# Performance work log

Hardware: AMD Instinct MI355X
Metric: run time of the kernel (lower is better)

Reference implementation:

```python
import jax, jax.numpy as jnp
import numpy as np

NUM_HEADS = 12
HEAD_DIM = 64
EPS = 1e-5


def _ln(t, g, b):
    m = t.mean(-1, keepdims=True)
    v = ((t - m) ** 2).mean(-1, keepdims=True)
    return (t - m) * jax.lax.rsqrt(v + EPS) * g + b


def _pool(t, conv_w, g, b, B, H, W, C):
    # t: [B, heads, 1+H*W, C] -> depthwise-conv pooled [B, heads, 1+Hp*Wp, C]
    cls = t[:, :, :1, :]
    sp = t[:, :, 1:, :].reshape(B * NUM_HEADS, H, W, C).transpose(0, 3, 1, 2)
    y = jax.lax.conv_general_dilated(
        sp, conv_w, (2, 2), [(1, 1), (1, 1)],
        feature_group_count=C,
        dimension_numbers=('NCHW', 'OIHW', 'NCHW'))
    Hp, Wp = y.shape[2], y.shape[3]
    y = y.reshape(B, NUM_HEADS, C, Hp * Wp).transpose(0, 1, 3, 2)
    y = jnp.concatenate([cls, y], axis=2)
    return _ln(y, g, b), (Hp, Wp)


def _rel_dist(q_s, k_s):
    q_ratio = max(k_s / q_s, 1.0)
    k_ratio = max(q_s / k_s, 1.0)
    d = jnp.arange(q_s)[:, None] * q_ratio - jnp.arange(k_s)[None, :] * k_ratio
    d = d + (k_s - 1) * k_ratio
    return d.astype(jnp.int32)


def _forward(x, pool_q_w, pool_k_w, pool_v_w,
             norm_q_g, norm_q_b, norm_k_g, norm_k_b, norm_v_g, norm_v_b,
             wq, bq, wk, bk, wv, bv, proj_w, proj_b,
             rel_pos_h, rel_pos_w, feat_h, feat_w):
    B, N, D = x.shape
    C = D // NUM_HEADS
    t = x.reshape(B, N, NUM_HEADS, C).transpose(0, 2, 1, 3)  # [B,h,N,C]
    q, (qh, qw) = _pool(t, pool_q_w, norm_q_g, norm_q_b, B, feat_h, feat_w, C)
    k, (kh, kw) = _pool(t, pool_k_w, norm_k_g, norm_k_b, B, feat_h, feat_w, C)
    v, _ = _pool(t, pool_v_w, norm_v_g, norm_v_b, B, feat_h, feat_w, C)

    def proj_heads(y, w, bias):
        n = y.shape[2]
        y = y.transpose(0, 2, 1, 3).reshape(B, n, D)
        y = y @ w + bias
        return y.reshape(B, n, NUM_HEADS, HEAD_DIM).transpose(0, 2, 1, 3)

    q = proj_heads(q, wq, bq)
    k = proj_heads(k, wk, bk)
    v = proj_heads(v, wv, bv)

    scale = HEAD_DIM ** -0.5
    attn = jnp.einsum('bhqd,bhkd->bhqk', q * scale, k)

    # spatial relative position bias (cal_rel_pos_type), cls token excluded
    Rh = rel_pos_h[_rel_dist(qh, kh)]   # [qh,kh,hd]
    Rw = rel_pos_w[_rel_dist(qw, kw)]   # [qw,kw,hd]
    r_q = q[:, :, 1:, :].reshape(B, NUM_HEADS, qh, qw, HEAD_DIM)
    rel_h = jnp.einsum('byhwc,hkc->byhwk', r_q, Rh)
    rel_w = jnp.einsum('byhwc,wkc->byhwk', r_q, Rw)
    bias2d = (rel_h[..., :, None] + rel_w[..., None, :]).reshape(
        B, NUM_HEADS, qh * qw, kh * kw)
    attn = attn.at[:, :, 1:, 1:].add(bias2d)

    attn = jax.nn.softmax(attn, axis=-1)
    out = jnp.einsum('bhqk,bhkd->bhqd', attn, v)
    out = out + q  # residual pooling
    out = out.transpose(0, 2, 1, 3).reshape(B, -1, NUM_HEADS * HEAD_DIM)
    return out @ proj_w + proj_b


def setup_inputs() -> dict:
    key = jax.random.key(0)
    ks = jax.random.split(key, 16)
    B, D, C = 16, 768, 64
    H = W = 56
    N = H * W + 1
    rs = 2 * 28 - 1
    rnd = lambda i, sh, s: jax.random.normal(ks[i], sh, jnp.float32) * s
    return {
        'x': rnd(0, (B, N, D), 1.0),
        'pool_q_w': rnd(1, (C, 1, 3, 3), 0.1),
        'pool_k_w': rnd(2, (C, 1, 3, 3), 0.1),
        'pool_v_w': rnd(3, (C, 1, 3, 3), 0.1),
        'norm_q_g': jnp.ones((C,), jnp.float32),
        'norm_q_b': jnp.zeros((C,), jnp.float32),
        'norm_k_g': jnp.ones((C,), jnp.float32),
        'norm_k_b': jnp.zeros((C,), jnp.float32),
        'norm_v_g': jnp.ones((C,), jnp.float32),
        'norm_v_b': jnp.zeros((C,), jnp.float32),
        'wq': rnd(4, (D, D), 0.02), 'bq': jnp.zeros((D,), jnp.float32),
        'wk': rnd(5, (D, D), 0.02), 'bk': jnp.zeros((D,), jnp.float32),
        'wv': rnd(6, (D, D), 0.02), 'bv': jnp.zeros((D,), jnp.float32),
        'proj_w': rnd(7, (D, D), 0.02), 'proj_b': jnp.zeros((D,), jnp.float32),
        'rel_pos_h': rnd(8, (rs, HEAD_DIM), 0.02),
        'rel_pos_w': rnd(9, (rs, HEAD_DIM), 0.02),
        'feat_h': 56, 'feat_w': 56,
    }


def reference(x, pool_q_w, pool_k_w, pool_v_w,
              norm_q_g, norm_q_b, norm_k_g, norm_k_b, norm_v_g, norm_v_b,
              wq, bq, wk, bk, wv, bv, proj_w, proj_b,
              rel_pos_h, rel_pos_w, feat_h, feat_w):
    return _forward(x, pool_q_w, pool_k_w, pool_v_w,
                    norm_q_g, norm_q_b, norm_k_g, norm_k_b,
                    norm_v_g, norm_v_b,
                    wq, bq, wk, bk, wv, bv, proj_w, proj_b,
                    rel_pos_h, rel_pos_w, int(feat_h), int(feat_w))
```

## Files before the change

### kernel.cpp

```cpp
#include <hip/hip_runtime.h>
#include <stdint.h>

#define NUM_HEADS 12
#define HEAD_DIM  64
#define HWDIM     56
#define PHDIM     28
#define NTOK      785
#define NIN       3137
#define BATCH     16
#define DMODEL    768
#define BHCNT     192
#define LOG2E     1.44269504f

typedef __attribute__((ext_vector_type(8))) short bf16x8;
typedef __attribute__((ext_vector_type(4))) short s16x4;
typedef __attribute__((ext_vector_type(4))) float f32x4;

static __device__ __forceinline__ float bf2f(short s) {
  unsigned u = ((unsigned)(unsigned short)s) << 16;
  float f; __builtin_memcpy(&f, &u, 4); return f;
}
static __device__ __forceinline__ short f2bf(float f) {
  unsigned u; __builtin_memcpy(&u, &f, 4);
  unsigned r = u + 0x7FFFu + ((u >> 16) & 1u);
  return (short)(r >> 16);
}
static __device__ __forceinline__ float fexp2(float x) {
#if defined(__has_builtin)
#if __has_builtin(__builtin_amdgcn_exp2f)
  return __builtin_amdgcn_exp2f(x);
#else
  return exp2f(x);
#endif
#else
  return exp2f(x);
#endif
}

static __device__ __forceinline__ int xcd_chunk(int orig, int nwg) {
  int xcd = orig & 7;
  int within = orig >> 3;
  int q = nwg >> 3, r = nwg & 7;
  int base = (xcd < r) ? xcd * (q + 1) : r * (q + 1) + (xcd - r) * q;
  return base + within;
}

#if defined(__has_builtin)
#if __has_builtin(__builtin_amdgcn_global_load_lds)
#define HAVE_GLLDS 1
#endif
#endif

static __device__ __forceinline__ void gl_lds16(const short* g, short* l) {
#ifdef HAVE_GLLDS
  __builtin_amdgcn_global_load_lds(
      (const __attribute__((address_space(1))) void*)g,
      (__attribute__((address_space(3))) void*)l, 16, 0, 0);
#else
  int lane = threadIdx.x & 63;
  *(bf16x8*)(l + lane * 8) = *(const bf16x8*)g;
#endif
}

__global__ __launch_bounds__(192) void pool_ln_kernel(
    const float* __restrict__ x,
    const float* __restrict__ wq9, const float* __restrict__ wk9, const float* __restrict__ wv9,
    const float* __restrict__ gq, const float* __restrict__ bq,
    const float* __restrict__ gk, const float* __restrict__ bk,
    const float* __restrict__ gv, const float* __restrict__ bv,
    short* __restrict__ Pq, short* __restrict__ Pk, short* __restrict__ Pv)
{
  __shared__ __align__(16) float wt_s[3][9][64];
  int tid = threadIdx.x;
  int blk = blockIdx.x;
  int b = blk / 197;
  int n0 = (blk - b * 197) * 4;

  for (int idx = tid; idx < 3 * 576; idx += 192) {
    int conv = idx / 576, rem = idx - conv * 576;
    int c = rem / 9, tap = rem - c * 9;
    const float* wsrc = (conv == 0) ? wq9 : (conv == 1) ? wk9 : wv9;
    wt_s[conv][tap][c] = wsrc[c * 9 + tap];
  }
  __syncthreads();

  int ch0 = tid * 4;
  int c4 = ch0 & 63;
  f32x4 g_q = *(const f32x4*)&gq[c4], b_q = *(const f32x4*)&bq[c4];
  f32x4 g_k = *(const f32x4*)&gk[c4], b_k = *(const f32x4*)&bk[c4];
  f32x4 g_v = *(const f32x4*)&gv[c4], b_v = *(const f32x4*)&bv[c4];

  for (int tt = 0; tt < 4; ++tt) {
    int n = n0 + tt;
    if (n >= NTOK) break;
    f32x4 aq = (f32x4){0.f, 0.f, 0.f, 0.f}, ak = aq, av = aq;
    if (n == 0) {
      f32x4 x4 = *(const f32x4*)&x[((size_t)b * NIN) * DMODEL + ch0];
      aq = ak = av = x4;
    } else {
      int s = n - 1;
      int i = s / PHDIM, j = s - i * PHDIM;
#pragma unroll
      for (int di = 0; di < 3; ++di) {
        int ii = 2 * i - 1 + di;
        if (ii < 0 || ii >= HWDIM) continue;
#pragma unroll
        for (int dj = 0; dj < 3; ++dj) {
          int jj = 2 * j - 1 + dj;
          if (jj < 0 || jj >= HWDIM) continue;
          f32x4 x4 = *(const f32x4*)&x[((size_t)b * NIN + 1 + ii * HWDIM + jj) * DMODEL + ch0];
          int tap = di * 3 + dj;
          f32x4 w0 = *(const f32x4*)&wt_s[0][tap][c4];
          f32x4 w1 = *(const f32x4*)&wt_s[1][tap][c4];
          f32x4 w2 = *(const f32x4*)&wt_s[2][tap][c4];
          aq += w0 * x4; ak += w1 * x4; av += w2 * x4;
        }
      }
    }
    size_t obase = ((size_t)b * NTOK + n) * DMODEL + ch0;
    {
      float sm = aq[0] + aq[1] + aq[2] + aq[3];
#pragma unroll
      for (int m = 1; m < 16; m <<= 1) sm += __shfl_xor(sm, m);
      float mn = sm * (1.f / 64.f);
      f32x4 d = aq - mn;
      float vs = d[0]*d[0] + d[1]*d[1] + d[2]*d[2] + d[3]*d[3];
#pragma unroll
      for (int m = 1; m < 16; m <<= 1) vs += __shfl_xor(vs, m);
      float rs = rsqrtf(vs * (1.f / 64.f) + 1e-5f);
      s16x4 o;
#pragma unroll
      for (int e = 0; e < 4; ++e) o[e] = f2bf(d[e] * rs * g_q[e] + b_q[e]);
      *(s16x4*)&Pq[obase] = o;
    }
    {
      float sm = ak[0] + ak[1] + ak[2] + ak[3];
#pragma unroll
      for (int m = 1; m < 16; m <<= 1) sm += __shfl_xor(sm, m);
      float mn = sm * (1.f / 64.f);
      f32x4 d = ak - mn;
      float vs = d[0]*d[0] + d[1]*d[1] + d[2]*d[2] + d[3]*d[3];
#pragma unroll
      for (int m = 1; m < 16; m <<= 1) vs += __shfl_xor(vs, m);
      float rs = rsqrtf(vs * (1.f / 64.f) + 1e-5f);
      s16x4 o;
#pragma unroll
      for (int e = 0; e < 4; ++e) o[e] = f2bf(d[e] * rs * g_k[e] + b_k[e]);
      *(s16x4*)&Pk[obase] = o;
    }
    {
      float sm = av[0] + av[1] + av[2] + av[3];
#pragma unroll
      for (int m = 1; m < 16; m <<= 1) sm += __shfl_xor(sm, m);
      float mn = sm * (1.f / 64.f);
      f32x4 d = av - mn;
      float vs = d[0]*d[0] + d[1]*d[1] + d[2]*d[2] + d[3]*d[3];
#pragma unroll
      for (int m = 1; m < 16; m <<= 1) vs += __shfl_xor(vs, m);
      float rs = rsqrtf(vs * (1.f / 64.f) + 1e-5f);
      s16x4 o;
#pragma unroll
      for (int e = 0; e < 4; ++e) o[e] = f2bf(d[e] * rs * g_v[e] + b_v[e]);
      *(s16x4*)&Pv[obase] = o;
    }
  }
}

__global__ __launch_bounds__(256) void trans_kernel(
    const float* __restrict__ s0, const float* __restrict__ s1,
    const float* __restrict__ s2, const float* __restrict__ s3,
    short* __restrict__ d0, short* __restrict__ d1,
    short* __restrict__ d2, short* __restrict__ d3)
{
  __shared__ float tile[32][33];
  int z = blockIdx.z;
  const float* s = (z == 0) ? s0 : (z == 1) ? s1 : (z == 2) ? s2 : s3;
  short* d = (z == 0) ? d0 : (z == 1) ? d1 : (z == 2) ? d2 : d3;
  int k0 = blockIdx.x * 32, n0 = blockIdx.y * 32;
  int tx = threadIdx.x, ty = threadIdx.y;
#pragma unroll
  for (int jj = 0; jj < 4; ++jj)
    tile[ty + jj * 8][tx] = s[(size_t)(k0 + ty + jj * 8) * DMODEL + n0 + tx];
  __syncthreads();
#pragma unroll
  for (int jj = 0; jj < 4; ++jj)
    d[(size_t)(n0 + ty + jj * 8) * DMODEL + k0 + tx] = f2bf(tile[tx][ty + jj * 8]);
}

static __device__ __forceinline__ void gemm_core(
    short* As, short* Bs,
    const short* __restrict__ A, const short* __restrict__ Bt,
    const float* __restrict__ bias, void* __restrict__ outp,
    int rowbase, int colbase, int M, int Nn, int mode)
{
  const int K = DMODEL;
  int tid = threadIdx.x;
  int wid = tid >> 6, lane = tid & 63;
  int lg = lane >> 4, lq = lane & 15;
  int wm = wid >> 1, wn = wid & 1;

  f32x4 acc[4][4];
#pragma unroll
  for (int i = 0; i < 4; ++i)
#pragma unroll
    for (int j = 0; j < 4; ++j) acc[i][j] = (f32x4){0.f, 0.f, 0.f, 0.f};

  int srow = tid >> 2;
  int scol = (tid & 3) * 8;
  int ar0 = min(rowbase + srow, M - 1);
  int ar1 = min(rowbase + 64 + srow, M - 1);
  int br0 = min(colbase + srow, Nn - 1);
  int br1 = min(colbase + 64 + srow, Nn - 1);
  const short* Ag0 = A + (size_t)ar0 * K + scol;
  const short* Ag1 = A + (size_t)ar1 * K + scol;
  const short* Bg0 = Bt + (size_t)br0 * K + scol;
  const short* Bg1 = Bt + (size_t)br1 * K + scol;

  auto stage = [&](int kt, int buf) __attribute__((always_inline)) {
    short* Ab = As + buf * 4096;
    short* Bb = Bs + buf * 4096;
    gl_lds16(Ag0 + kt, Ab + wid * 512);
    gl_lds16(Ag1 + kt, Ab + 2048 + wid * 512);
    gl_lds16(Bg0 + kt, Bb + wid * 512);
    gl_lds16(Bg1 + kt, Bb + 2048 + wid * 512);
  };

  stage(0, 0);
  __syncthreads();
  int cur = 0;
  for (int kt = 0; kt < K; kt += 32) {
    if (kt + 32 < K) stage(kt + 32, cur ^ 1);
    const short* Ac = As + cur * 4096;
    const short* Bc = Bs + cur * 4096;
    bf16x8 aFrag[4], bFrag[4];
#pragma unroll
    for (int mi = 0; mi < 4; ++mi)
      aFrag[mi] = *(const bf16x8*)&Ac[(wm * 64 + mi * 16 + lq) * 32 + lg * 8];
#pragma unroll
    for (int ni = 0; ni < 4; ++ni)
      bFrag[ni] = *(const bf16x8*)&Bc[(wn * 64 + ni * 16 + lq) * 32 + lg * 8];
    __builtin_amdgcn_s_setprio(1);
#pragma unroll
    for (int mi = 0; mi < 4; ++mi)
#pragma unroll
      for (int ni = 0; ni < 4; ++ni)
        acc[mi][ni] = __builtin_amdgcn_mfma_f32_16x16x32_bf16(aFrag[mi], bFrag[ni], acc[mi][ni], 0, 0, 0);
    __builtin_amdgcn_s_setprio(0);
    __syncthreads();
    cur ^= 1;
  }

#pragma unroll
  for (int mi = 0; mi < 4; ++mi) {
    int rowq = rowbase + wm * 64 + mi * 16 + lg * 4;
#pragma unroll
    for (int r = 0; r < 4; ++r) {
      int row = rowq + r;
      if (row < M) {
        if (mode == 2) {
          float bb = bias[row];
#pragma unroll
          for (int ni = 0; ni < 4; ++ni) {
            int col = colbase + wn * 64 + ni * 16 + lq;
            if (col < Nn) {
              int b = col / NTOK, n = col - b * NTOK;
              float v = acc[mi][ni][r] + bb;
              ((short*)outp)[((size_t)b * DMODEL + row) * NTOK + n] = f2bf(v);
            }
          }
        } else {
          int bb = row / NTOK;
          int nn = row - bb * NTOK;
#pragma unroll
          for (int ni = 0; ni < 4; ++ni) {
            int col = colbase + wn * 64 + ni * 16 + lq;
            float v = acc[mi][ni][r] + bias[col];
            if (mode == 0) {
              ((float*)outp)[(size_t)row * DMODEL + col] = v;
            } else {
              ((short*)outp)[(((size_t)(bb * NUM_HEADS + (col >> 6)) * NTOK + nn) << 6) + (col & 63)] = f2bf(v);
            }
          }
        }
      }
    }
  }
}

__global__ __launch_bounds__(256) void gemm_qkv_kernel(
    const short* __restrict__ Pq, const short* __restrict__ WqT,
    const float* __restrict__ bq, short* __restrict__ qhd,
    const short* __restrict__ Pk, const short* __restrict__ WkT,
    const float* __restrict__ bk, short* __restrict__ khd,
    const short* __restrict__ WvT, const short* __restrict__ Pv,
    const float* __restrict__ bv, short* __restrict__ vtg)
{
  __shared__ short As[2 * 4096];
  __shared__ short Bs[2 * 4096];
  const int NWG = 1782;
  int lid = xcd_chunk(blockIdx.x, NWG);
  if (lid < 1188) {
    int which = lid / 594;
    int sub = lid - which * 594;
    int rowbase = (sub / 6) * 128;
    int colbase = (sub % 6) * 128;
    gemm_core(As, Bs,
              which ? Pk : Pq, which ? WkT : WqT,
              which ? bk : bq, which ? (void*)khd : (void*)qhd,
              rowbase, colbase, BATCH * NTOK, DMODEL, 1);
  } else {
    int sub = lid - 1188;
    int rowbase = (sub % 6) * 128;
    int colbase = (sub / 6) * 128;
    gemm_core(As, Bs, WvT, Pv, bv, (void*)vtg,
              rowbase, colbase, DMODEL, BATCH * NTOK, 2);
  }
}

__global__ __launch_bounds__(256) void gemm_proj_kernel(
    const short* __restrict__ Afin, const short* __restrict__ WpT,
    const float* __restrict__ bp, float* __restrict__ outp)
{
  __shared__ short As[2 * 4096];
  __shared__ short Bs[2 * 4096];
  const int NWG = 594;
  int lid = xcd_chunk(blockIdx.x, NWG);
  int rowbase = (lid / 6) * 128;
  int colbase = (lid % 6) * 128;
  gemm_core(As, Bs, Afin, WpT, bp, (void*)outp,
            rowbase, colbase, BATCH * NTOK, DMODEL, 0);
}

__global__ __launch_bounds__(256) void relbias_kernel(
    const short* __restrict__ qh, const float* __restrict__ rph,
    const float* __restrict__ rpw, short* __restrict__ RelHt, short* __restrict__ RelWt)
{
  int line = blockIdx.x;
  int bh = blockIdx.y;
  int mode = blockIdx.z;
  __shared__ __align__(16) float qt_s[28 * 68];
  __shared__ __align__(16) float rt_s[28 * 68];
  int tid = threadIdx.x;
  const float* rp = (mode == 0) ? rph : rpw;
  for (int idx = tid; idx < 28 * 64; idx += 256) {
    int rr = idx >> 6, c = idx & 63;
    int qi = (mode == 0) ? (1 + line * PHDIM + rr) : (1 + rr * PHDIM + line);
    qt_s[rr * 68 + c] = bf2f(qh[((size_t)bh * NTOK + qi) * HEAD_DIM + c]);
    rt_s[rr * 68 + c] = rp[(line - rr + 27) * HEAD_DIM + c];
  }
  __syncthreads();
  short* dst = (mode == 0) ? RelHt : RelWt;
  for (int o = tid; o < 784; o += 256) {
    int kk = o / PHDIM, rr = o - kk * PHDIM;
    const f32x4* qa = (const f32x4*)&qt_s[rr * 68];
    const f32x4* ra = (const f32x4*)&rt_s[kk * 68];
    f32x4 a4 = (f32x4){0.f, 0.f, 0.f, 0.f};
#pragma unroll
    for (int i = 0; i < 16; ++i) a4 += qa[i] * ra[i];
    float s = (a4[0] + a4[1] + a4[2] + a4[3]) * LOG2E;
    int qrow = (mode == 0) ? (line * PHDIM + rr) : (rr * PHDIM + line);
    dst[((size_t)bh * PHDIM + kk) * 784 + qrow] = f2bf(s);
  }
}

__global__ __launch_bounds__(256) void flash5_kernel(
    const short* __restrict__ qh, const short* __restrict__ kh, const short* __restrict__ vtg,
    const short* __restrict__ RelHt, const short* __restrict__ RelWt,
    short* __restrict__ Afin)
{
  int id = blockIdx.x;
  int slot = id >> 3;
  int bh = (id & 7) * 24 + slot / 13;
  int qt = slot - (slot / 13) * 13;
  int qbase = qt * 64;
  int tid = threadIdx.x, wid = tid >> 6, lane = tid & 63;
  int lg = lane >> 4, lq = lane & 15;

  __shared__ __align__(16) short ks[64 * 64];
  __shared__ __align__(16) short vt[64 * 64];
  __shared__ __align__(16) float relh_t[28][64];
  __shared__ __align__(16) float relw_t[28][64];
  __shared__ __align__(16) float axl[4][16];

  for (int idx = tid; idx < 28 * 64; idx += 256) {
    int kk = idx >> 6, ql = idx & 63;
    int qi = qbase + ql;
    float rh = 0.f, rw = 0.f;
    if (qi >= 1 && qi < NTOK) {
      rh = bf2f(RelHt[((size_t)bh * PHDIM + kk) * 784 + qi - 1]);
      rw = bf2f(RelWt[((size_t)bh * PHDIM + kk) * 784 + qi - 1]);
    }
    relh_t[kk][ql] = rh; relw_t[kk][ql] = rw;
  }

  int qi0 = qbase + wid * 16 + lq;
  int qiq = min(qi0, NTOK - 1);
  const short* qrow = qh + ((size_t)bh * NTOK + qiq) * HEAD_DIM;
  bf16x8 bq0 = *(const bf16x8*)(qrow + lg * 8);
  bf16x8 bq1 = *(const bf16x8*)(qrow + 32 + lg * 8);

  float m_l = -3e30f, l_l = 0.f;
  f32x4 acc[4];
#pragma unroll
  for (int ch = 0; ch < 4; ++ch) acc[ch] = (f32x4){0.f, 0.f, 0.f, 0.f};

  const float scale2 = 0.125f * LOG2E;
  int q_local = wid * 16 + lq;
  const short* kbase = kh + (size_t)bh * NTOK * HEAD_DIM;
  const short* vbase = vtg + (size_t)bh * (size_t)HEAD_DIM * NTOK;

  int c0 = tid, c1 = 256 + tid;
  int rr0 = c0 >> 3, j0 = c0 & 7;
  int rr1 = c1 >> 3, j1 = c1 & 7;
  int koff0 = ((rr0 & 15) >> 2) * 16 + (rr0 >> 4) * 4 + (rr0 & 3);
  int koff1 = ((rr1 & 15) >> 2) * 16 + (rr1 >> 4) * 4 + (rr1 & 3);
  int ksw0 = (j0 ^ (rr0 & 7)) << 3;
  int ksw1 = (j1 ^ (rr1 & 7)) << 3;
  int vsw0 = (j0 ^ (rr0 & 7)) << 3;
  int vsw1 = (j1 ^ (rr1 & 7)) << 3;
  const short* vsrc0 = vbase + (size_t)rr0 * NTOK + vsw0;
  const short* vsrc1 = vbase + (size_t)rr1 * NTOK + vsw1;

  auto step_body = [&](int kvb, bool first, bool last) __attribute__((always_inline)) {
    __syncthreads();
    gl_lds16(kbase + (size_t)min(kvb + koff0, NTOK - 1) * HEAD_DIM + ksw0, ks + wid * 512);
    gl_lds16(kbase + (size_t)min(kvb + koff1, NTOK - 1) * HEAD_DIM + ksw1, ks + 2048 + wid * 512);
    gl_lds16(vsrc0 + kvb, vt + wid * 512);
    gl_lds16(vsrc1 + kvb, vt + 2048 + wid * 512);
    __syncthreads();

    int base = kvb + 16 * lg;
    int km1 = base - 1;
    int t = max(km1, 0);
    int ki = t / PHDIM;
    int kj = t - ki * PHDIM;
    if (km1 < 0) kj = -1;

    float p[16];
#pragma unroll
    for (int kt = 0; kt < 4; ++kt) {
      int kl = kt * 16 + lq;
      const char* kp = (const char*)ks + kl * 128;
      int swz = kl & 7;
      bf16x8 aK0 = *(const bf16x8*)(kp + ((lg ^ swz) << 4));
      bf16x8 aK1 = *(const bf16x8*)(kp + (((lg + 4) ^ swz) << 4));
      f32x4 s = (f32x4){0.f, 0.f, 0.f, 0.f};
      __builtin_amdgcn_s_setprio(1);
      s = __builtin_amdgcn_mfma_f32_16x16x32_bf16(aK0, bq0, s, 0, 0, 0);
      s = __builtin_amdgcn_mfma_f32_16x16x32_bf16(aK1, bq1, s, 0, 0, 0);
      __builtin_amdgcn_s_setprio(0);
#pragma unroll
      for (int r = 0; r < 4; ++r) {
        int i = kt * 4 + r;
        float v = s[r] * scale2;
        if (first) {
          int key = base + i;
          if (key >= 1) v += relh_t[ki][q_local] + relw_t[kj][q_local];
        } else if (last) {
          int key = base + i;
          v += relh_t[ki][q_local] + relw_t[kj][q_local];
          if (key >= NTOK) v = -3e30f;
        } else {
          v += relh_t[ki][q_local] + relw_t[kj][q_local];
        }
        p[i] = v;
        ++kj;
        if (kj == PHDIM) { kj = 0; ++ki; }
      }
    }

    float pm = p[0];
#pragma unroll
    for (int i = 1; i < 16; ++i) pm = fmaxf(pm, p[i]);
    pm = fmaxf(pm, __shfl_xor(pm, 16));
    pm = fmaxf(pm, __shfl_xor(pm, 32));
    if (!__all(pm - m_l <= 11.5f)) {
      float mnew = fmaxf(m_l, pm);
      float alpha = fexp2(m_l - mnew);
      m_l = mnew;
      l_l *= alpha;
      if (lg == 0) axl[wid][lq] = alpha;
      f32x4 av = *(const f32x4*)&axl[wid][lg * 4];
#pragma unroll
      for (int ch = 0; ch < 4; ++ch)
#pragma unroll
        for (int r = 0; r < 4; ++r) acc[ch][r] *= av[r];
    }
    float ps = 0.f;
#pragma unroll
    for (int i = 0; i < 16; ++i) { p[i] = fexp2(p[i] - m_l); ps += p[i]; }
    ps += __shfl_xor(ps, 16);
    ps += __shfl_xor(ps, 32);
    l_l += ps;

    bf16x8 pa0, pa1;
#pragma unroll
    for (int j = 0; j < 4; ++j) {
      unsigned u0, u1, v0, v1;
      __builtin_memcpy(&u0, &p[2 * j], 4);
      __builtin_memcpy(&u1, &p[2 * j + 1], 4);
      __builtin_memcpy(&v0, &p[8 + 2 * j], 4);
      __builtin_memcpy(&v1, &p[8 + 2 * j + 1], 4);
      ((unsigned*)&pa0)[j] = (u0 >> 16) | (u1 & 0xFFFF0000u);
      ((unsigned*)&pa1)[j] = (v0 >> 16) | (v1 & 0xFFFF0000u);
    }
    __builtin_amdgcn_s_setprio(1);
#pragma unroll
    for (int ch = 0; ch < 4; ++ch) {
      int d = ch * 16 + lq;
      const char* vrow = (const char*)vt + d * 128;
      int swz = lq & 7;
      bf16x8 bv0 = *(const bf16x8*)(vrow + (((2 * lg + 0) ^ swz) << 4));
      bf16x8 bv1 = *(const bf16x8*)(vrow + (((2 * lg + 1) ^ swz) << 4));
      acc[ch] = __builtin_amdgcn_mfma_f32_16x16x32_bf16(pa0, bv0, acc[ch], 0, 0, 0);
      acc[ch] = __builtin_amdgcn_mfma_f32_16x16x32_bf16(pa1, bv1, acc[ch], 0, 0, 0);
    }
    __builtin_amdgcn_s_setprio(0);
  };

  step_body(0, true, false);
  for (int step = 1; step < 12; ++step) step_body(step * 64, false, false);
  step_body(12 * 64, false, true);

  if (lg == 0) axl[wid][lq] = l_l;
  f32x4 lv = *(const f32x4*)&axl[wid][lg * 4];
  int b = bh / NUM_HEADS, h = bh - b * NUM_HEADS;
#pragma unroll
  for (int r = 0; r < 4; ++r) {
    int qi = qbase + wid * 16 + lg * 4 + r;
    if (qi < NTOK) {
      float inv = 1.f / lv[r];
#pragma unroll
      for (int ch = 0; ch < 4; ++ch) {
        int d = ch * 16 + lq;
        float o = acc[ch][r] * inv + bf2f(qh[((size_t)bh * NTOK + qi) * HEAD_DIM + d]);
        Afin[((size_t)b * NTOK + qi) * DMODEL + h * HEAD_DIM + d] = f2bf(o);
      }
    }
  }
}

extern "C" void kernel_launch(void* const* d_in, const int* in_sizes, int n_in,
                              void* d_out, int out_size, void* d_ws, size_t ws_size,
                              hipStream_t stream)
{
  (void)in_sizes; (void)n_in; (void)out_size; (void)ws_size;
  const float* x   = (const float*)d_in[0];
  const float* pqw = (const float*)d_in[1];
  const float* pkw = (const float*)d_in[2];
  const float* pvw = (const float*)d_in[3];
  const float* gq  = (const float*)d_in[4];
  const float* bq_ = (const float*)d_in[5];
  const float* gk  = (const float*)d_in[6];
  const float* bk_ = (const float*)d_in[7];
  const float* gv  = (const float*)d_in[8];
  const float* bv_ = (const float*)d_in[9];
  const float* wq  = (const float*)d_in[10];
  const float* bqp = (const float*)d_in[11];
  const float* wk  = (const float*)d_in[12];
  const float* bkp = (const float*)d_in[13];
  const float* wv  = (const float*)d_in[14];
  const float* bvp = (const float*)d_in[15];
  const float* wp  = (const float*)d_in[16];
  const float* bpp = (const float*)d_in[17];
  const float* rph = (const float*)d_in[18];
  const float* rpw = (const float*)d_in[19];

  char* ws = (char*)d_ws;
  size_t off = 0;
  auto alloc = [&](size_t bytes) -> void* {
    void* p = ws + off; off += (bytes + 255) & ~(size_t)255; return p;
  };
  const size_t MROWS = (size_t)BATCH * NTOK;
  short* Pq  = (short*)alloc(MROWS * DMODEL * 2);
  short* Pk  = (short*)alloc(MROWS * DMODEL * 2);
  short* Pv  = (short*)alloc(MROWS * DMODEL * 2);
  short* WqT = (short*)alloc((size_t)DMODEL * DMODEL * 2);
  short* WkT = (short*)alloc((size_t)DMODEL * DMODEL * 2);
  short* WvT = (short*)alloc((size_t)DMODEL * DMODEL * 2);
  short* WpT = (short*)alloc((size_t)DMODEL * DMODEL * 2);
  short* qhd = (short*)alloc(MROWS * DMODEL * 2 + 4096);
  short* khd = (short*)alloc(MROWS * DMODEL * 2 + 4096);
  short* vtg = (short*)alloc(MROWS * DMODEL * 2 + 8192);
  short* RelHt = (short*)alloc((size_t)BHCNT * 784 * 28 * 2);
  short* RelWt = (short*)alloc((size_t)BHCNT * 784 * 28 * 2);
  short* Afin = (short*)alloc(MROWS * DMODEL * 2);

  pool_ln_kernel<<<dim3(16 * 197), 192, 0, stream>>>(
      x, pqw, pkw, pvw, gq, bq_, gk, bk_, gv, bv_, Pq, Pk, Pv);
  trans_kernel<<<dim3(24, 24, 4), dim3(32, 8), 0, stream>>>(
      wq, wk, wv, wp, WqT, WkT, WvT, WpT);
  gemm_qkv_kernel<<<dim3(1782), 256, 0, stream>>>(
      Pq, WqT, bqp, qhd, Pk, WkT, bkp, khd, WvT, Pv, bvp, vtg);
  relbias_kernel<<<dim3(28, BHCNT, 2), 256, 0, stream>>>(qhd, rph, rpw, RelHt, RelWt);
  flash5_kernel<<<dim3(2496), 256, 0, stream>>>(qhd, khd, vtg, RelHt, RelWt, Afin);
  gemm_proj_kernel<<<dim3(594), 256, 0, stream>>>(Afin, WpT, bpp, (float*)d_out);
}
```

Baseline: 370.0 us.

## Double-buffer K/V tiles in attention and deepen GEMM prefetch with explicit waitcnts

The attention kernel gets two LDS buffers for K and V, so the next 64-key tile streams in while the current one is processed. Explicit vmcnt waits and raw barriers replace the two full __syncthreads per step. The shared GEMM mainloop now keeps two stages in flight and issues the next stage after the fragment loads, using partial vmcnt waits. This hides global-to-LDS latency but doubles the attention LDS footprint, which may lower occupancy, and the hand-counted waitcnts are fragile.

```diff
diff --git a/kernel.cpp b/kernel.cpp
--- a/kernel.cpp
+++ b/kernel.cpp
@@ -226,10 +226,17 @@
   };
 
   stage(0, 0);
-  __syncthreads();
+  stage(32, 1);
   int cur = 0;
   for (int kt = 0; kt < K; kt += 32) {
-    if (kt + 32 < K) stage(kt + 32, cur ^ 1);
+    if (kt + 32 < K) {
+      asm volatile("s_waitcnt vmcnt(4)" ::: "memory");
+    } else {
+      asm volatile("s_waitcnt vmcnt(0)" ::: "memory");
+    }
+    __builtin_amdgcn_sched_barrier(0);
+    __builtin_amdgcn_s_barrier();
+    __builtin_amdgcn_sched_barrier(0);
     const short* Ac = As + cur * 4096;
     const short* Bc = Bs + cur * 4096;
     bf16x8 aFrag[4], bFrag[4];
@@ -239,6 +246,10 @@
 #pragma unroll
     for (int ni = 0; ni < 4; ++ni)
       bFrag[ni] = *(const bf16x8*)&Bc[(wn * 64 + ni * 16 + lq) * 32 + lg * 8];
+    asm volatile("s_waitcnt lgkmcnt(0)" ::: "memory");
+    __builtin_amdgcn_sched_barrier(0);
+    __builtin_amdgcn_s_barrier();
+    if (kt + 64 < K) stage(kt + 64, cur);
     __builtin_amdgcn_s_setprio(1);
 #pragma unroll
     for (int mi = 0; mi < 4; ++mi)
@@ -246,7 +257,6 @@
       for (int ni = 0; ni < 4; ++ni)
         acc[mi][ni] = __builtin_amdgcn_mfma_f32_16x16x32_bf16(aFrag[mi], bFrag[ni], acc[mi][ni], 0, 0, 0);
     __builtin_amdgcn_s_setprio(0);
-    __syncthreads();
     cur ^= 1;
   }
 
@@ -363,7 +373,7 @@
   }
 }
 
-__global__ __launch_bounds__(256) void flash5_kernel(
+__global__ __launch_bounds__(256) void flash6_kernel(
     const short* __restrict__ qh, const short* __restrict__ kh, const short* __restrict__ vtg,
     const short* __restrict__ RelHt, const short* __restrict__ RelWt,
     short* __restrict__ Afin)
@@ -376,8 +386,8 @@
   int tid = threadIdx.x, wid = tid >> 6, lane = tid & 63;
   int lg = lane >> 4, lq = lane & 15;
 
-  __shared__ __align__(16) short ks[64 * 64];
-  __shared__ __align__(16) short vt[64 * 64];
+  __shared__ __align__(16) short ks[2][64 * 64];
+  __shared__ __align__(16) short vt[2][64 * 64];
   __shared__ __align__(16) float relh_t[28][64];
   __shared__ __align__(16) float relw_t[28][64];
   __shared__ __align__(16) float axl[4][16];
@@ -421,26 +431,43 @@
   const short* vsrc0 = vbase + (size_t)rr0 * NTOK + vsw0;
   const short* vsrc1 = vbase + (size_t)rr1 * NTOK + vsw1;
 
-  auto step_body = [&](int kvb, bool first, bool last) __attribute__((always_inline)) {
-    __syncthreads();
-    gl_lds16(kbase + (size_t)min(kvb + koff0, NTOK - 1) * HEAD_DIM + ksw0, ks + wid * 512);
-    gl_lds16(kbase + (size_t)min(kvb + koff1, NTOK - 1) * HEAD_DIM + ksw1, ks + 2048 + wid * 512);
-    gl_lds16(vsrc0 + kvb, vt + wid * 512);
-    gl_lds16(vsrc1 + kvb, vt + 2048 + wid * 512);
-    __syncthreads();
+  auto stage = [&](int t, int buf) __attribute__((always_inline)) {
+    int kvb = t * 64;
+    gl_lds16(kbase + (size_t)min(kvb + koff0, NTOK - 1) * HEAD_DIM + ksw0, ks[buf] + wid * 512);
+    gl_lds16(kbase + (size_t)min(kvb + koff1, NTOK - 1) * HEAD_DIM + ksw1, ks[buf] + 2048 + wid * 512);
+    gl_lds16(vsrc0 + kvb, vt[buf] + wid * 512);
+    gl_lds16(vsrc1 + kvb, vt[buf] + 2048 + wid * 512);
+  };
+
+  stage(0, 0);
+  asm volatile("s_waitcnt lgkmcnt(0)" ::: "memory");
+
+  auto step_body = [&](int t, bool first, bool last) __attribute__((always_inline)) {
+    int kvb = t * 64;
+    int buf = t & 1;
+    __builtin_amdgcn_s_barrier();
+    if (!last) stage(t + 1, buf ^ 1);
+    if (!last) { asm volatile("s_waitcnt vmcnt(4)" ::: "memory"); }
+    else       { asm volatile("s_waitcnt vmcnt(0)" ::: "memory"); }
+    __builtin_amdgcn_sched_barrier(0);
+    __builtin_amdgcn_s_barrier();
+    __builtin_amdgcn_sched_barrier(0);
 
     int base = kvb + 16 * lg;
     int km1 = base - 1;
-    int t = max(km1, 0);
-    int ki = t / PHDIM;
-    int kj = t - ki * PHDIM;
+    int tt = max(km1, 0);
+    int ki = tt / PHDIM;
+    int kj = tt - ki * PHDIM;
     if (km1 < 0) kj = -1;
+
+    const short* ksb = ks[buf];
+    const short* vtb = vt[buf];
 
     float p[16];
 #pragma unroll
     for (int kt = 0; kt < 4; ++kt) {
       int kl = kt * 16 + lq;
-      const char* kp = (const char*)ks + kl * 128;
+      const char* kp = (const char*)ksb + kl * 128;
       int swz = kl & 7;
       bf16x8 aK0 = *(const bf16x8*)(kp + ((lg ^ swz) << 4));
       bf16x8 aK1 = *(const bf16x8*)(kp + (((lg + 4) ^ swz) << 4));
@@ -508,7 +535,7 @@
 #pragma unroll
     for (int ch = 0; ch < 4; ++ch) {
       int d = ch * 16 + lq;
-      const char* vrow = (const char*)vt + d * 128;
+      const char* vrow = (const char*)vtb + d * 128;
       int swz = lq & 7;
       bf16x8 bv0 = *(const bf16x8*)(vrow + (((2 * lg + 0) ^ swz) << 4));
       bf16x8 bv1 = *(const bf16x8*)(vrow + (((2 * lg + 1) ^ swz) << 4));
@@ -519,8 +546,8 @@
   };
 
   step_body(0, true, false);
-  for (int step = 1; step < 12; ++step) step_body(step * 64, false, false);
-  step_body(12 * 64, false, true);
+  for (int step = 1; step < 12; ++step) step_body(step, false, false);
+  step_body(12, false, true);
 
   if (lg == 0) axl[wid][lq] = l_l;
   f32x4 lv = *(const f32x4*)&axl[wid][lg * 4];
@@ -593,6 +620,6 @@
   gemm_qkv_kernel<<<dim3(1782), 256, 0, stream>>>(
       Pq, WqT, bqp, qhd, Pk, WkT, bkp, khd, WvT, Pv, bvp, vtg);
   relbias_kernel<<<dim3(28, BHCNT, 2), 256, 0, stream>>>(qhd, rph, rpw, RelHt, RelWt);
-  flash5_kernel<<<dim3(2496), 256, 0, stream>>>(qhd, khd, vtg, RelHt, RelWt, Afin);
+  flash6_kernel<<<dim3(2496), 256, 0, stream>>>(qhd, khd, vtg, RelHt, RelWt, Afin);
   gemm_proj_kernel<<<dim3(594), 256, 0, stream>>>(Afin, WpT, bpp, (float*)d_out);
 }
```

Result: slower. 378.2 us (+2.2%).

## Fold relative position bias into QK matmul via augmented Q/K vectors

Applied to the files above, without the earlier changes.

Q is pre-scaled and extended to 128 dims, with the 28 rel_h and 28 rel_w bias values written into the extra slots. K is extended with one-hot indicators for each key's row and column, so the bias comes out of the MFMA dot product. This removes the per-element LDS bias lookups and index arithmetic from the flash inner loop. In exchange it doubles the K tile loads and QK MFMAs, adds two new kernels, and writes two large augmented buffers. Bias values are now rounded to bf16 in the MFMA operand path.

```diff
diff --git a/kernel.cpp b/kernel.cpp
--- a/kernel.cpp
+++ b/kernel.cpp
@@ -331,9 +331,48 @@
             rowbase, colbase, BATCH * NTOK, DMODEL, 0);
 }
 
+__global__ __launch_bounds__(256) void qaug_kernel(
+    const short* __restrict__ qh, short* __restrict__ qaug)
+{
+  int t = threadIdx.x;
+  size_t gr = (size_t)blockIdx.x * 16 + (t >> 4);
+  int c = t & 15;
+  bf16x8 o = {0, 0, 0, 0, 0, 0, 0, 0};
+  if (c < 8) {
+    bf16x8 v = *(const bf16x8*)(qh + gr * 64 + c * 8);
+    const float s2 = 0.125f * LOG2E;
+#pragma unroll
+    for (int e = 0; e < 8; ++e) o[e] = f2bf(bf2f(v[e]) * s2);
+  }
+  *(bf16x8*)(qaug + gr * 128 + c * 8) = o;
+}
+
+__global__ __launch_bounds__(256) void kaug_kernel(
+    const short* __restrict__ kh, short* __restrict__ kaug)
+{
+  int t = threadIdx.x;
+  size_t gr = (size_t)blockIdx.x * 16 + (t >> 4);
+  int c = t & 15;
+  int n = (int)(gr % NTOK);
+  bf16x8 o = {0, 0, 0, 0, 0, 0, 0, 0};
+  if (c < 8) {
+    o = *(const bf16x8*)(kh + gr * 64 + c * 8);
+  } else if (n >= 1) {
+    int km1 = n - 1;
+    int ki = km1 / PHDIM, kj = km1 - (km1 / PHDIM) * PHDIM;
+    int d0 = c * 8;
+#pragma unroll
+    for (int e = 0; e < 8; ++e) {
+      int d = d0 + e;
+      o[e] = (d == 64 + ki || d == 92 + kj) ? (short)0x3F80 : (short)0;
+    }
+  }
+  *(bf16x8*)(kaug + gr * 128 + c * 8) = o;
+}
+
 __global__ __launch_bounds__(256) void relbias_kernel(
     const short* __restrict__ qh, const float* __restrict__ rph,
-    const float* __restrict__ rpw, short* __restrict__ RelHt, short* __restrict__ RelWt)
+    const float* __restrict__ rpw, short* __restrict__ qaug)
 {
   int line = blockIdx.x;
   int bh = blockIdx.y;
@@ -349,7 +388,6 @@
     rt_s[rr * 68 + c] = rp[(line - rr + 27) * HEAD_DIM + c];
   }
   __syncthreads();
-  short* dst = (mode == 0) ? RelHt : RelWt;
   for (int o = tid; o < 784; o += 256) {
     int kk = o / PHDIM, rr = o - kk * PHDIM;
     const f32x4* qa = (const f32x4*)&qt_s[rr * 68];
@@ -358,14 +396,15 @@
 #pragma unroll
     for (int i = 0; i < 16; ++i) a4 += qa[i] * ra[i];
     float s = (a4[0] + a4[1] + a4[2] + a4[3]) * LOG2E;
-    int qrow = (mode == 0) ? (line * PHDIM + rr) : (rr * PHDIM + line);
-    dst[((size_t)bh * PHDIM + kk) * 784 + qrow] = f2bf(s);
-  }
-}
-
-__global__ __launch_bounds__(256) void flash5_kernel(
-    const short* __restrict__ qh, const short* __restrict__ kh, const short* __restrict__ vtg,
-    const short* __restrict__ RelHt, const short* __restrict__ RelWt,
+    int qi = (mode == 0) ? (1 + line * PHDIM + rr) : (1 + rr * PHDIM + line);
+    int dim = (mode == 0) ? (64 + kk) : (92 + kk);
+    qaug[((size_t)bh * NTOK + qi) * 128 + dim] = f2bf(s);
+  }
+}
+
+__global__ __launch_bounds__(256) void flash7_kernel(
+    const short* __restrict__ qaug, const short* __restrict__ qh,
+    const short* __restrict__ kaug, const short* __restrict__ vtg,
     short* __restrict__ Afin)
 {
   int id = blockIdx.x;
@@ -376,96 +415,72 @@
   int tid = threadIdx.x, wid = tid >> 6, lane = tid & 63;
   int lg = lane >> 4, lq = lane & 15;
 
-  __shared__ __align__(16) short ks[64 * 64];
+  __shared__ __align__(16) short ks[64 * 128];
   __shared__ __align__(16) short vt[64 * 64];
-  __shared__ __align__(16) float relh_t[28][64];
-  __shared__ __align__(16) float relw_t[28][64];
   __shared__ __align__(16) float axl[4][16];
-
-  for (int idx = tid; idx < 28 * 64; idx += 256) {
-    int kk = idx >> 6, ql = idx & 63;
-    int qi = qbase + ql;
-    float rh = 0.f, rw = 0.f;
-    if (qi >= 1 && qi < NTOK) {
-      rh = bf2f(RelHt[((size_t)bh * PHDIM + kk) * 784 + qi - 1]);
-      rw = bf2f(RelWt[((size_t)bh * PHDIM + kk) * 784 + qi - 1]);
-    }
-    relh_t[kk][ql] = rh; relw_t[kk][ql] = rw;
-  }
 
   int qi0 = qbase + wid * 16 + lq;
   int qiq = min(qi0, NTOK - 1);
-  const short* qrow = qh + ((size_t)bh * NTOK + qiq) * HEAD_DIM;
-  bf16x8 bq0 = *(const bf16x8*)(qrow + lg * 8);
-  bf16x8 bq1 = *(const bf16x8*)(qrow + 32 + lg * 8);
+  const short* qrow = qaug + ((size_t)bh * NTOK + qiq) * 128;
+  bf16x8 bq[4];
+#pragma unroll
+  for (int c = 0; c < 4; ++c) bq[c] = *(const bf16x8*)(qrow + c * 32 + lg * 8);
 
   float m_l = -3e30f, l_l = 0.f;
   f32x4 acc[4];
 #pragma unroll
   for (int ch = 0; ch < 4; ++ch) acc[ch] = (f32x4){0.f, 0.f, 0.f, 0.f};
 
-  const float scale2 = 0.125f * LOG2E;
-  int q_local = wid * 16 + lq;
-  const short* kbase = kh + (size_t)bh * NTOK * HEAD_DIM;
+  const short* kbase = kaug + (size_t)bh * NTOK * 128;
   const short* vbase = vtg + (size_t)bh * (size_t)HEAD_DIM * NTOK;
 
+  int koffK[4], kslot[4];
+#pragma unroll
+  for (int m = 0; m < 4; ++m) {
+    int c = m * 256 + tid;
+    int rr = c >> 4, j = c & 15;
+    koffK[m] = ((rr & 15) >> 2) * 16 + (rr >> 4) * 4 + (rr & 3);
+    kslot[m] = (j ^ (rr & 15)) << 3;
+  }
   int c0 = tid, c1 = 256 + tid;
-  int rr0 = c0 >> 3, j0 = c0 & 7;
-  int rr1 = c1 >> 3, j1 = c1 & 7;
-  int koff0 = ((rr0 & 15) >> 2) * 16 + (rr0 >> 4) * 4 + (rr0 & 3);
-  int koff1 = ((rr1 & 15) >> 2) * 16 + (rr1 >> 4) * 4 + (rr1 & 3);
-  int ksw0 = (j0 ^ (rr0 & 7)) << 3;
-  int ksw1 = (j1 ^ (rr1 & 7)) << 3;
-  int vsw0 = (j0 ^ (rr0 & 7)) << 3;
-  int vsw1 = (j1 ^ (rr1 & 7)) << 3;
-  const short* vsrc0 = vbase + (size_t)rr0 * NTOK + vsw0;
-  const short* vsrc1 = vbase + (size_t)rr1 * NTOK + vsw1;
-
-  auto step_body = [&](int kvb, bool first, bool last) __attribute__((always_inline)) {
+  int vr0 = c0 >> 3, vj0 = c0 & 7;
+  int vr1 = c1 >> 3, vj1 = c1 & 7;
+  const short* vsrc0 = vbase + (size_t)vr0 * NTOK + ((vj0 ^ (vr0 & 7)) << 3);
+  const short* vsrc1 = vbase + (size_t)vr1 * NTOK + ((vj1 ^ (vr1 & 7)) << 3);
+
+  auto step_body = [&](int kvb, bool last) __attribute__((always_inline)) {
     __syncthreads();
-    gl_lds16(kbase + (size_t)min(kvb + koff0, NTOK - 1) * HEAD_DIM + ksw0, ks + wid * 512);
-    gl_lds16(kbase + (size_t)min(kvb + koff1, NTOK - 1) * HEAD_DIM + ksw1, ks + 2048 + wid * 512);
+#pragma unroll
+    for (int m = 0; m < 4; ++m)
+      gl_lds16(kbase + (size_t)min(kvb + koffK[m], NTOK - 1) * 128 + kslot[m],
+               ks + m * 2048 + wid * 512);
     gl_lds16(vsrc0 + kvb, vt + wid * 512);
     gl_lds16(vsrc1 + kvb, vt + 2048 + wid * 512);
     __syncthreads();
 
-    int base = kvb + 16 * lg;
-    int km1 = base - 1;
-    int t = max(km1, 0);
-    int ki = t / PHDIM;
-    int kj = t - ki * PHDIM;
-    if (km1 < 0) kj = -1;
-
     float p[16];
 #pragma unroll
     for (int kt = 0; kt < 4; ++kt) {
       int kl = kt * 16 + lq;
-      const char* kp = (const char*)ks + kl * 128;
-      int swz = kl & 7;
-      bf16x8 aK0 = *(const bf16x8*)(kp + ((lg ^ swz) << 4));
-      bf16x8 aK1 = *(const bf16x8*)(kp + (((lg + 4) ^ swz) << 4));
+      const char* kp = (const char*)ks + kl * 256;
+      int swz = kl & 15;
       f32x4 s = (f32x4){0.f, 0.f, 0.f, 0.f};
       __builtin_amdgcn_s_setprio(1);
-      s = __builtin_amdgcn_mfma_f32_16x16x32_bf16(aK0, bq0, s, 0, 0, 0);
-      s = __builtin_amdgcn_mfma_f32_16x16x32_bf16(aK1, bq1, s, 0, 0, 0);
+#pragma unroll
+      for (int c = 0; c < 4; ++c) {
+        bf16x8 aK = *(const bf16x8*)(kp + (((c * 4 + lg) ^ swz) << 4));
+        s = __builtin_amdgcn_mfma_f32_16x16x32_bf16(aK, bq[c], s, 0, 0, 0);
+      }
       __builtin_amdgcn_s_setprio(0);
 #pragma unroll
       for (int r = 0; r < 4; ++r) {
         int i = kt * 4 + r;
-        float v = s[r] * scale2;
-        if (first) {
-          int key = base + i;
-          if (key >= 1) v += relh_t[ki][q_local] + relw_t[kj][q_local];
-        } else if (last) {
-          int key = base + i;
-          v += relh_t[ki][q_local] + relw_t[kj][q_local];
+        float v = s[r];
+        if (last) {
+          int key = kvb + 16 * lg + i;
           if (key >= NTOK) v = -3e30f;
-        } else {
-          v += relh_t[ki][q_local] + relw_t[kj][q_local];
         }
         p[i] = v;
-        ++kj;
-        if (kj == PHDIM) { kj = 0; ++ki; }
       }
     }
 
@@ -518,9 +533,8 @@
     __builtin_amdgcn_s_setprio(0);
   };
 
-  step_body(0, true, false);
-  for (int step = 1; step < 12; ++step) step_body(step * 64, false, false);
-  step_body(12 * 64, false, true);
+  for (int step = 0; step < 12; ++step) step_body(step * 64, false);
+  step_body(12 * 64, true);
 
   if (lg == 0) axl[wid][lq] = l_l;
   f32x4 lv = *(const f32x4*)&axl[wid][lg * 4];
@@ -582,8 +596,8 @@
   short* qhd = (short*)alloc(MROWS * DMODEL * 2 + 4096);
   short* khd = (short*)alloc(MROWS * DMODEL * 2 + 4096);
   short* vtg = (short*)alloc(MROWS * DMODEL * 2 + 8192);
-  short* RelHt = (short*)alloc((size_t)BHCNT * 784 * 28 * 2);
-  short* RelWt = (short*)alloc((size_t)BHCNT * 784 * 28 * 2);
+  short* qaug = (short*)alloc((size_t)BHCNT * NTOK * 128 * 2 + 8192);
+  short* kaug = (short*)alloc((size_t)BHCNT * NTOK * 128 * 2 + 8192);
   short* Afin = (short*)alloc(MROWS * DMODEL * 2);
 
   pool_ln_kernel<<<dim3(16 * 197), 192, 0, stream>>>(
@@ -592,7 +606,9 @@
       wq, wk, wv, wp, WqT, WkT, WvT, WpT);
   gemm_qkv_kernel<<<dim3(1782), 256, 0, stream>>>(
       Pq, WqT, bqp, qhd, Pk, WkT, bkp, khd, WvT, Pv, bvp, vtg);
-  relbias_kernel<<<dim3(28, BHCNT, 2), 256, 0, stream>>>(qhd, rph, rpw, RelHt, RelWt);
-  flash5_kernel<<<dim3(2496), 256, 0, stream>>>(qhd, khd, vtg, RelHt, RelWt, Afin);
+  qaug_kernel<<<dim3(9420), 256, 0, stream>>>(qhd, qaug);
+  kaug_kernel<<<dim3(9420), 256, 0, stream>>>(khd, kaug);
+  relbias_kernel<<<dim3(28, BHCNT, 2), 256, 0, stream>>>(qhd, rph, rpw, qaug);
+  flash7_kernel<<<dim3(2496), 256, 0, stream>>>(qaug, qhd, kaug, vtg, Afin);
   gemm_proj_kernel<<<dim3(594), 256, 0, stream>>>(Afin, WpT, bpp, (float*)d_out);
 }
```

Measured after the change: 376.7 us. About the same (+1.8%).
